# Optimization experiments

Hardware: AMD Instinct MI355X
Metric: run time of the kernel (lower is better)

The kernel has to match this reference:

```python
import jax, jax.numpy as jnp
import numpy as np

TOP_K = 5
EPS = 1e-12

def _l2norm(x, axis=-1):
    n = jnp.sqrt(jnp.sum(x * x, axis=axis, keepdims=True))
    return x / jnp.maximum(n, EPS)

def setup_inputs() -> dict:
    key = jax.random.key(0)
    ks = jax.random.split(key, 6)
    B, S, D, N = 16, 2048, 512, 200000
    return {
        "hidden_states": jax.random.normal(ks[0], (B, S, D), dtype=jnp.float32),
        "doc_embeddings": jax.random.normal(ks[1], (N, D), dtype=jnp.float32),
        "W_q": jax.random.normal(ks[2], (D, D), dtype=jnp.float32) * 0.02,
        "b_q": jnp.zeros((D,), dtype=jnp.float32),
        "W_gate": jax.random.normal(ks[3], (D, 2 * D), dtype=jnp.float32) * 0.02,
        "b_gate": jnp.zeros((D,), dtype=jnp.float32),
    }

def reference(hidden_states, doc_embeddings, W_q, b_q, W_gate, b_gate):
    B, S, D = hidden_states.shape
    # set_doc_embeddings: cosine metric normalizes doc table once
    docs = _l2norm(doc_embeddings, axis=1)          # [N, D]
    # forward: mean-pool query, linear encode
    query = hidden_states.mean(axis=1)              # [B, D]
    query = query @ W_q.T + b_q                     # torch Linear: x @ W^T + b
    # cosine similarity scan over full corpus
    q = _l2norm(query, axis=1)                      # [B, D]
    scores_full = q @ docs.T                        # [B, N]  (memory-bound scan)
    top_scores, indices = jax.lax.top_k(scores_full, TOP_K)  # [B, K], [B, K]
    # fuse context (gate method)
    retrieved = docs[indices]                       # [B, K, D] gather
    weights = jax.nn.softmax(top_scores, axis=1)    # [B, K]
    context = jnp.einsum('bk,bkd->bd', weights, retrieved)   # [B, D]
    context_exp = jnp.broadcast_to(context[:, None, :], (B, S, D))
    combined = jnp.concatenate([hidden_states, context_exp], axis=-1)  # [B, S, 2D]
    gate = jax.nn.sigmoid(combined @ W_gate.T + b_gate)       # [B, S, D]
    fused = gate * hidden_states + (1.0 - gate) * context_exp
    return top_scores, indices, fused
```

## Files before the change

kernel.cpp:

```cpp
#include <hip/hip_runtime.h>
#include <hip/hip_bf16.h>
#include <math.h>

#define BB 16
#define SS 2048
#define DD 512
#define NDOCS 200000
#define TOPK 5
#define EPSN 1e-12f
#define NEG_INF (-3.0e38f)

#define TILE_N 128
#define KC 32
#define NCHUNK (DD / KC)
#define NBLK3 ((NDOCS + TILE_N - 1) / TILE_N)

typedef short s16x8 __attribute__((ext_vector_type(8)));
typedef float f32x4 __attribute__((ext_vector_type(4)));

__device__ __forceinline__ short f2bf(float f) {
    __bf16 b = (__bf16)f;
    short s;
    __builtin_memcpy(&s, &b, 2);
    return s;
}

__device__ __forceinline__ void gload_lds16(const void* g, void* l) {
    __builtin_amdgcn_global_load_lds(
        (const __attribute__((address_space(1))) void*)g,
        (__attribute__((address_space(3))) void*)l, 16, 0, 0);
}

__global__ __launch_bounds__(128) void k1_mean_partial(
    const float* __restrict__ hs, float* __restrict__ partial) {
    int b = blockIdx.y, sc = blockIdx.x;
    int t = threadIdx.x;
    const float4* src = (const float4*)(hs + (size_t)(b * SS + sc * 64) * DD);
    float4 acc = {0.f, 0.f, 0.f, 0.f};
    for (int s = 0; s < 64; ++s) {
        float4 v = src[(size_t)s * 128 + t];
        acc.x += v.x; acc.y += v.y; acc.z += v.z; acc.w += v.w;
    }
    ((float4*)partial)[(size_t)(sc * BB + b) * 128 + t] = acc;
}

__global__ __launch_bounds__(128) void k1b_mean_reduce(
    const float* __restrict__ partial, float* __restrict__ mean) {
    int b = blockIdx.y, jc = blockIdx.x;
    int j = jc * 128 + threadIdx.x;
    float s = 0.f;
    for (int c = 0; c < 32; ++c) s += partial[(size_t)(c * BB + b) * DD + j];
    mean[(size_t)b * DD + j] = s * (1.0f / 2048.0f);
}

__global__ __launch_bounds__(256) void k2a_q_gemv(
    const float* __restrict__ mean, const float* __restrict__ Wq,
    const float* __restrict__ bq, float* __restrict__ qtmp) {
    int b = blockIdx.y, jc = blockIdx.x;
    int t = threadIdx.x;
    int r = t >> 4, c = t & 15;
    int row = jc * 16 + r;
    const float4* wr = (const float4*)(Wq + (size_t)row * DD);
    const float4* mv = (const float4*)(mean + (size_t)b * DD);
    float acc = 0.f;
#pragma unroll
    for (int it = 0; it < 8; ++it) {
        int k4 = c + it * 16;
        float4 w = wr[k4], m = mv[k4];
        acc = fmaf(w.x, m.x, acc); acc = fmaf(w.y, m.y, acc);
        acc = fmaf(w.z, m.z, acc); acc = fmaf(w.w, m.w, acc);
    }
#pragma unroll
    for (int m = 1; m < 16; m <<= 1) acc += __shfl_xor(acc, m);
    if (c == 0) qtmp[(size_t)b * DD + row] = acc + bq[row];
}

__global__ __launch_bounds__(256) void k2b_q_norm(
    const float* __restrict__ qtmp, float* __restrict__ qv) {
    int b = blockIdx.x, t = threadIdx.x;
    __shared__ float red[4];
    float a0 = qtmp[(size_t)b * DD + t];
    float a1 = qtmp[(size_t)b * DD + t + 256];
    float ss = a0 * a0 + a1 * a1;
#pragma unroll
    for (int m = 1; m < 64; m <<= 1) ss += __shfl_xor(ss, m);
    if ((t & 63) == 0) red[t >> 6] = ss;
    __syncthreads();
    float inv = 1.0f / fmaxf(sqrtf(red[0] + red[1] + red[2] + red[3]), EPSN);
    qv[(size_t)b * DD + t] = a0 * inv;
    qv[(size_t)b * DD + t + 256] = a1 * inv;
}

__global__ __launch_bounds__(256) void k2c_qsplit(
    const float* __restrict__ qv, short* __restrict__ qsplit) {
    int b = blockIdx.x, t = threadIdx.x;
#pragma unroll
    for (int kk = 0; kk < 2; ++kk) {
        int k = t + kk * 256;
        float f = qv[(size_t)b * DD + k];
        unsigned u = __float_as_uint(f);
        short hi = (short)(u >> 16);
        float r = f - __uint_as_float(u & 0xFFFF0000u);
        short lo = f2bf(r);
        int slot = k >> 3, j = k & 7;
        int off = b * 512 + ((slot ^ (b & 7)) << 3) + j;
        qsplit[off] = hi;
        qsplit[8192 + off] = lo;
    }
}

__global__ __launch_bounds__(256) void k3_scores(
    const float* __restrict__ docs, const short* __restrict__ qsplit,
    float* __restrict__ cand_s, int* __restrict__ cand_i) {
    __shared__ float4 Et[2][TILE_N * 8];
    __shared__ short qS[2 * 8192];

    int t = threadIdx.x;
    int w = t >> 6, lane = t & 63;
    int bq = lane & 15, kg = lane >> 4;
    int blk = blockIdx.x;
    long tileBase = (long)blk * TILE_N;

#pragma unroll
    for (int j = 0; j < 8; ++j) {
        int u = ((w * 8 + j) << 6) + lane;
        gload_lds16(qsplit + (size_t)u * 8, (void*)&qS[(w * 8 + j) * 512]);
    }

    auto stage = [&](int c, int buf) {
#pragma unroll
        for (int j = 0; j < 4; ++j) {
            int u = ((w * 4 + j) << 6) + lane;
            int n = u >> 3, slot = u & 7;
            int k4src = slot ^ (n & 7);
            long row = tileBase + n;
            if (row > NDOCS - 1) row = NDOCS - 1;
            gload_lds16(docs + row * (long)DD + c * KC + k4src * 4,
                        (void*)&Et[buf][(w * 4 + j) * 64]);
        }
    };

    f32x4 acc[2], n1[2], n2[2];
#pragma unroll
    for (int f = 0; f < 2; ++f) {
        acc[f] = (f32x4){0.f, 0.f, 0.f, 0.f};
        n1[f]  = (f32x4){0.f, 0.f, 0.f, 0.f};
        n2[f]  = (f32x4){0.f, 0.f, 0.f, 0.f};
    }

    stage(0, 0);
    for (int c = 0; c < NCHUNK; ++c) {
        __syncthreads();
        if (c + 1 < NCHUNK) stage(c + 1, (c + 1) & 1);

        int qphys = ((c * 4 + kg) ^ (bq & 7)) << 3;
        s16x8 qh = *(const s16x8*)&qS[bq * 512 + qphys];
        s16x8 ql = *(const s16x8*)&qS[8192 + bq * 512 + qphys];

        const float4* Eb = &Et[c & 1][0];
#pragma unroll
        for (int f = 0; f < 2; ++f) {
            int d = (w << 5) + (f << 4) + bq;
            int base = d << 3;
            float4 e0 = Eb[base + ((kg * 2) ^ (d & 7))];
            float4 e1 = Eb[base + ((kg * 2 + 1) ^ (d & 7))];
            float ef[8] = {e0.x, e0.y, e0.z, e0.w, e1.x, e1.y, e1.z, e1.w};
            s16x8 ah, al;
#pragma unroll
            for (int i = 0; i < 8; ++i) {
                unsigned u = __float_as_uint(ef[i]);
                ah[i] = (short)(u >> 16);
                al[i] = f2bf(ef[i] - __uint_as_float(u & 0xFFFF0000u));
            }
            acc[f] = __builtin_amdgcn_mfma_f32_16x16x32_bf16(ah, qh, acc[f], 0, 0, 0);
            acc[f] = __builtin_amdgcn_mfma_f32_16x16x32_bf16(ah, ql, acc[f], 0, 0, 0);
            acc[f] = __builtin_amdgcn_mfma_f32_16x16x32_bf16(al, qh, acc[f], 0, 0, 0);
            n1[f]  = __builtin_amdgcn_mfma_f32_16x16x32_bf16(ah, ah, n1[f], 0, 0, 0);
            n2[f]  = __builtin_amdgcn_mfma_f32_16x16x32_bf16(ah, al, n2[f], 0, 0, 0);
        }
    }

    float* Sb = (float*)&Et[0][0];
#pragma unroll
    for (int f = 0; f < 2; ++f) {
        int rd = bq & 3;
        float nd = n1[f][rd] + 2.0f * n2[f][rd];
        float invn = 1.0f / fmaxf(sqrtf(nd), EPSN);
#pragma unroll
        for (int r = 0; r < 4; ++r) {
            float iv = __shfl(invn, kg * 20 + r);
            int n = (w << 5) + (f << 4) + (kg << 2) + r;
            Sb[bq * TILE_N + n] = acc[f][r] * iv;
        }
    }
    __syncthreads();

    for (int jj = 0; jj < 4; ++jj) {
        int b = w * 4 + jj;
        float v[2]; int nn[2];
#pragma unroll
        for (int m = 0; m < 2; ++m) {
            int n = lane + m * 64;
            nn[m] = n;
            v[m] = (tileBase + n < NDOCS) ? Sb[b * TILE_N + n] : NEG_INF;
        }
        for (int r = 0; r < TOPK; ++r) {
            float bv = v[0]; int bi = nn[0];
            if (v[1] > bv || (v[1] == bv && nn[1] < bi)) { bv = v[1]; bi = nn[1]; }
#pragma unroll
            for (int mm = 1; mm < 64; mm <<= 1) {
                float ov = __shfl_xor(bv, mm);
                int   oi = __shfl_xor(bi, mm);
                if (ov > bv || (ov == bv && oi < bi)) { bv = ov; bi = oi; }
            }
            if (lane == 0) {
                cand_s[((long)blk * BB + b) * TOPK + r] = bv;
                cand_i[((long)blk * BB + b) * TOPK + r] = (int)(tileBase + bi);
            }
#pragma unroll
            for (int m = 0; m < 2; ++m)
                if (nn[m] == bi) v[m] = NEG_INF;
        }
    }
}

__global__ __launch_bounds__(256) void k4a_topk_ctx(
    const float* __restrict__ docs, const float* __restrict__ cand_s,
    const int* __restrict__ cand_i, float* __restrict__ ctx,
    float* __restrict__ outp) {
    int b = blockIdx.x, t = threadIdx.x;
    __shared__ float sv[256];
    __shared__ int   si[256];
    __shared__ float topv[TOPK];
    __shared__ int   topi[TOPK];
    __shared__ float red[4];
    __shared__ float nrm5[TOPK];
    __shared__ float wts[TOPK];

    float lv[TOPK]; int li[TOPK];
#pragma unroll
    for (int r = 0; r < TOPK; ++r) { lv[r] = NEG_INF; li[r] = 0x7fffffff; }

    for (int j = t; j < NBLK3 * TOPK; j += 256) {
        int blk = j / TOPK, r = j - blk * TOPK;
        float s = cand_s[(long)blk * (BB * TOPK) + b * TOPK + r];
        int  di = cand_i[(long)blk * (BB * TOPK) + b * TOPK + r];
        if (s > lv[TOPK - 1] || (s == lv[TOPK - 1] && di < li[TOPK - 1])) {
            lv[TOPK - 1] = s; li[TOPK - 1] = di;
#pragma unroll
            for (int k = TOPK - 1; k > 0; --k) {
                if (lv[k] > lv[k - 1] || (lv[k] == lv[k - 1] && li[k] < li[k - 1])) {
                    float tv = lv[k]; lv[k] = lv[k - 1]; lv[k - 1] = tv;
                    int   ti = li[k]; li[k] = li[k - 1]; li[k - 1] = ti;
                }
            }
        }
    }

    int p = 0;
    for (int r = 0; r < TOPK; ++r) {
        float hv = (p < TOPK) ? lv[p] : NEG_INF;
        int   hi = (p < TOPK) ? li[p] : 0x7fffffff;
        sv[t] = hv; si[t] = hi;
        __syncthreads();
        for (int off = 128; off > 0; off >>= 1) {
            if (t < off) {
                float ov = sv[t + off]; int oi = si[t + off];
                if (ov > sv[t] || (ov == sv[t] && oi < si[t])) { sv[t] = ov; si[t] = oi; }
            }
            __syncthreads();
        }
        if (t == 0) { topv[r] = sv[0]; topi[r] = si[0]; }
        __syncthreads();
        if (hv == topv[r] && hi == topi[r]) ++p;
        __syncthreads();
    }

    for (int r = 0; r < TOPK; ++r) {
        const float* dr = docs + (size_t)topi[r] * DD;
        float s2 = dr[t] * dr[t] + dr[t + 256] * dr[t + 256];
#pragma unroll
        for (int m = 1; m < 64; m <<= 1) s2 += __shfl_xor(s2, m);
        if ((t & 63) == 0) red[t >> 6] = s2;
        __syncthreads();
        if (t == 0) nrm5[r] = sqrtf(red[0] + red[1] + red[2] + red[3]);
        __syncthreads();
    }

    if (t == 0) {
        float m = topv[0];
        float e[TOPK], s = 0.f;
#pragma unroll
        for (int r = 0; r < TOPK; ++r) { e[r] = expf(topv[r] - m); s += e[r]; }
#pragma unroll
        for (int r = 0; r < TOPK; ++r) wts[r] = e[r] / s;
    }
    __syncthreads();

    for (int j = t; j < DD; j += 256) {
        float c = 0.f;
#pragma unroll
        for (int r = 0; r < TOPK; ++r)
            c += wts[r] * docs[(size_t)topi[r] * DD + j] / fmaxf(nrm5[r], EPSN);
        ctx[(size_t)b * DD + j] = c;
    }

    if (t < TOPK) {
        outp[b * TOPK + t] = topv[t];
        outp[BB * TOPK + b * TOPK + t] = (float)topi[t];
    }
}

__global__ __launch_bounds__(256) void k4b_ctxb_gemv(
    const float* __restrict__ ctx, const float* __restrict__ Wg,
    const float* __restrict__ bgt, float* __restrict__ ctxb) {
    int b = blockIdx.y, jc = blockIdx.x;
    int t = threadIdx.x;
    int r = t >> 4, c = t & 15;
    int row = jc * 16 + r;
    const float4* wr = (const float4*)(Wg + (size_t)row * (2 * DD) + DD);
    const float4* mv = (const float4*)(ctx + (size_t)b * DD);
    float acc = 0.f;
#pragma unroll
    for (int it = 0; it < 8; ++it) {
        int k4 = c + it * 16;
        float4 w = wr[k4], m = mv[k4];
        acc = fmaf(w.x, m.x, acc); acc = fmaf(w.y, m.y, acc);
        acc = fmaf(w.z, m.z, acc); acc = fmaf(w.w, m.w, acc);
    }
#pragma unroll
    for (int m = 1; m < 16; m <<= 1) acc += __shfl_xor(acc, m);
    if (c == 0) ctxb[(size_t)b * DD + row] = acc + bgt[row];
}

#define BK 32
__global__ __launch_bounds__(512, 2) void k5_gemm_fused(
    const float* __restrict__ hs, const float* __restrict__ Wg,
    const float* __restrict__ ctx, const float* __restrict__ ctxb,
    float* __restrict__ outF) {
    __shared__ short At[128][BK];
    __shared__ short Bt[512][BK];
    __shared__ float ctxLds[DD];
    __shared__ float ctxbLds[DD];

    int bm = blockIdx.x;
    int t = threadIdx.x;
    int wv = t >> 6, lane = t & 63, ln = lane & 15, kg = lane >> 4;
    int wm = (wv >> 2) * 64, wn = (wv & 3) * 128;
    int bbatch = bm >> 4;

    ctxLds[t]  = ctx[(size_t)bbatch * DD + t];
    ctxbLds[t] = ctxb[(size_t)bbatch * DD + t];

    float4 pf[5][2];
    auto gload = [&](int kt) {
        {
            const float* src = hs + (size_t)(bm * 128 + (t >> 2)) * DD + kt * BK + (t & 3) * 8;
            pf[0][0] = ((const float4*)src)[0];
            pf[0][1] = ((const float4*)src)[1];
        }
#pragma unroll
        for (int i = 0; i < 4; ++i) {
            int u = t + i * 512;
            const float* src = Wg + (size_t)(u >> 2) * (2 * DD) + kt * BK + (u & 3) * 8;
            pf[1 + i][0] = ((const float4*)src)[0];
            pf[1 + i][1] = ((const float4*)src)[1];
        }
    };
    auto cvt1 = [&](float4 lo, float4 hi) {
        s16x8 cv;
        cv[0] = f2bf(lo.x); cv[1] = f2bf(lo.y); cv[2] = f2bf(lo.z); cv[3] = f2bf(lo.w);
        cv[4] = f2bf(hi.x); cv[5] = f2bf(hi.y); cv[6] = f2bf(hi.z); cv[7] = f2bf(hi.w);
        return cv;
    };
    auto cvtwrite = [&]() {
        {
            int row = t >> 2, slot = t & 3;
            int sl = slot ^ ((row >> 1) & 3);
            *(s16x8*)(&At[row][sl * 8]) = cvt1(pf[0][0], pf[0][1]);
        }
#pragma unroll
        for (int i = 0; i < 4; ++i) {
            int u = t + i * 512;
            int row = u >> 2, slot = u & 3;
            int sl = slot ^ ((row >> 1) & 3);
            *(s16x8*)(&Bt[row][sl * 8]) = cvt1(pf[1 + i][0], pf[1 + i][1]);
        }
    };

    f32x4 accv[4][8];
#pragma unroll
    for (int i = 0; i < 4; ++i)
#pragma unroll
        for (int j = 0; j < 8; ++j) accv[i][j] = (f32x4){0.f, 0.f, 0.f, 0.f};

    gload(0);
    for (int kt = 0; kt < DD / BK; ++kt) {
        __syncthreads();
        cvtwrite();
        if (kt + 1 < DD / BK) gload(kt + 1);
        __syncthreads();
        s16x8 af[4], bfr[8];
#pragma unroll
        for (int mi = 0; mi < 4; ++mi) {
            int row = wm + mi * 16 + ln;
            int sl = kg ^ ((row >> 1) & 3);
            af[mi] = *(const s16x8*)&At[row][sl * 8];
        }
#pragma unroll
        for (int nj = 0; nj < 8; ++nj) {
            int row = wn + nj * 16 + ln;
            int sl = kg ^ ((row >> 1) & 3);
            bfr[nj] = *(const s16x8*)&Bt[row][sl * 8];
        }
#pragma unroll
        for (int mi = 0; mi < 4; ++mi)
#pragma unroll
            for (int nj = 0; nj < 8; ++nj)
                accv[mi][nj] = __builtin_amdgcn_mfma_f32_16x16x32_bf16(
                    af[mi], bfr[nj], accv[mi][nj], 0, 0, 0);
    }

#pragma unroll
    for (int mi = 0; mi < 4; ++mi)
#pragma unroll
        for (int nj = 0; nj < 8; ++nj)
#pragma unroll
            for (int r = 0; r < 4; ++r) {
                int ri = wm + mi * 16 + kg * 4 + r;
                int ci = wn + nj * 16 + ln;
                size_t grow = (size_t)bm * 128 + ri;
                float logit = accv[mi][nj][r] + ctxbLds[ci];
                float g = __builtin_amdgcn_rcpf(1.0f + __expf(-logit));
                float h = hs[grow * DD + ci];
                float cx = ctxLds[ci];
                outF[grow * DD + ci] = g * h + (1.0f - g) * cx;
            }
}

extern "C" void kernel_launch(void* const* d_in, const int* in_sizes, int n_in,
                              void* d_out, int out_size, void* d_ws, size_t ws_size,
                              hipStream_t stream) {
    const float* hs   = (const float*)d_in[0];
    const float* docs = (const float*)d_in[1];
    const float* Wq   = (const float*)d_in[2];
    const float* bq   = (const float*)d_in[3];
    const float* Wg   = (const float*)d_in[4];
    const float* bgt  = (const float*)d_in[5];
    float* outp = (float*)d_out;
    float* ws = (float*)d_ws;

    float* partial = ws;
    float* mean    = partial + 32 * BB * DD;
    float* qtmp    = mean + BB * DD;
    float* qv      = qtmp + BB * DD;
    float* ctx     = qv + BB * DD;
    float* ctxb    = ctx + BB * DD;
    float* cand_s  = ctxb + BB * DD;
    int*   cand_i  = (int*)(cand_s + NBLK3 * BB * TOPK);
    short* qsplit  = (short*)(cand_i + NBLK3 * BB * TOPK);

    k1_mean_partial<<<dim3(32, BB), 128, 0, stream>>>(hs, partial);
    k1b_mean_reduce<<<dim3(4, BB), 128, 0, stream>>>(partial, mean);
    k2a_q_gemv<<<dim3(32, BB), 256, 0, stream>>>(mean, Wq, bq, qtmp);
    k2b_q_norm<<<BB, 256, 0, stream>>>(qtmp, qv);
    k2c_qsplit<<<BB, 256, 0, stream>>>(qv, qsplit);
    k3_scores<<<NBLK3, 256, 0, stream>>>(docs, qsplit, cand_s, cand_i);
    k4a_topk_ctx<<<BB, 256, 0, stream>>>(docs, cand_s, cand_i, ctx, outp);
    k4b_ctxb_gemv<<<dim3(32, BB), 256, 0, stream>>>(ctx, Wg, bgt, ctxb);
    k5_gemm_fused<<<256, 512, 0, stream>>>(hs, Wg, ctx, ctxb,
                                           outp + 2 * BB * TOPK);
}
```

Baseline: 256.0 us.

## Make k3 persistent per-wave with register doc loads and running top-k

```diff
diff --git a/kernel.cpp b/kernel.cpp
--- a/kernel.cpp
+++ b/kernel.cpp
@@ -10,10 +10,8 @@
 #define EPSN 1e-12f
 #define NEG_INF (-3.0e38f)
 
-#define TILE_N 128
-#define KC 32
-#define NCHUNK (DD / KC)
-#define NBLK3 ((NDOCS + TILE_N - 1) / TILE_N)
+#define NW 4096
+#define NTILE 12500
 
 typedef short s16x8 __attribute__((ext_vector_type(8)));
 typedef float f32x4 __attribute__((ext_vector_type(4)));
@@ -109,61 +107,51 @@
     }
 }
 
-__global__ __launch_bounds__(256) void k3_scores(
+__global__ __launch_bounds__(256, 4) void k3_scores(
     const float* __restrict__ docs, const short* __restrict__ qsplit,
     float* __restrict__ cand_s, int* __restrict__ cand_i) {
-    __shared__ float4 Et[2][TILE_N * 8];
     __shared__ short qS[2 * 8192];
 
     int t = threadIdx.x;
     int w = t >> 6, lane = t & 63;
     int bq = lane & 15, kg = lane >> 4;
-    int blk = blockIdx.x;
-    long tileBase = (long)blk * TILE_N;
 
 #pragma unroll
     for (int j = 0; j < 8; ++j) {
         int u = ((w * 8 + j) << 6) + lane;
         gload_lds16(qsplit + (size_t)u * 8, (void*)&qS[(w * 8 + j) * 512]);
     }
-
-    auto stage = [&](int c, int buf) {
-#pragma unroll
-        for (int j = 0; j < 4; ++j) {
-            int u = ((w * 4 + j) << 6) + lane;
-            int n = u >> 3, slot = u & 7;
-            int k4src = slot ^ (n & 7);
-            long row = tileBase + n;
-            if (row > NDOCS - 1) row = NDOCS - 1;
-            gload_lds16(docs + row * (long)DD + c * KC + k4src * 4,
-                        (void*)&Et[buf][(w * 4 + j) * 64]);
+    __syncthreads();
+
+    int gw = blockIdx.x * 4 + w;
+
+    float lv[TOPK]; int li[TOPK];
+#pragma unroll
+    for (int r = 0; r < TOPK; ++r) { lv[r] = NEG_INF; li[r] = 0x7fffffff; }
+
+    auto ins = [&](float s, int di) {
+        if (s > lv[4] || (s == lv[4] && di < li[4])) {
+            lv[4] = s; li[4] = di;
+#pragma unroll
+            for (int k = 4; k > 0; --k) {
+                if (lv[k] > lv[k - 1] || (lv[k] == lv[k - 1] && li[k] < li[k - 1])) {
+                    float tv = lv[k]; lv[k] = lv[k - 1]; lv[k - 1] = tv;
+                    int   ti = li[k]; li[k] = li[k - 1]; li[k - 1] = ti;
+                }
+            }
         }
     };
 
-    f32x4 acc[2], n1[2], n2[2];
-#pragma unroll
-    for (int f = 0; f < 2; ++f) {
-        acc[f] = (f32x4){0.f, 0.f, 0.f, 0.f};
-        n1[f]  = (f32x4){0.f, 0.f, 0.f, 0.f};
-        n2[f]  = (f32x4){0.f, 0.f, 0.f, 0.f};
-    }
-
-    stage(0, 0);
-    for (int c = 0; c < NCHUNK; ++c) {
-        __syncthreads();
-        if (c + 1 < NCHUNK) stage(c + 1, (c + 1) & 1);
-
-        int qphys = ((c * 4 + kg) ^ (bq & 7)) << 3;
-        s16x8 qh = *(const s16x8*)&qS[bq * 512 + qphys];
-        s16x8 ql = *(const s16x8*)&qS[8192 + bq * 512 + qphys];
-
-        const float4* Eb = &Et[c & 1][0];
-#pragma unroll
-        for (int f = 0; f < 2; ++f) {
-            int d = (w << 5) + (f << 4) + bq;
-            int base = d << 3;
-            float4 e0 = Eb[base + ((kg * 2) ^ (d & 7))];
-            float4 e1 = Eb[base + ((kg * 2 + 1) ^ (d & 7))];
+    for (int tt = gw; tt < NTILE; tt += NW) {
+        const float4* dp = (const float4*)docs + (size_t)(tt * 16 + bq) * 128 + kg * 2;
+        f32x4 acc = {0.f, 0.f, 0.f, 0.f};
+        f32x4 n1  = {0.f, 0.f, 0.f, 0.f};
+        f32x4 n2  = {0.f, 0.f, 0.f, 0.f};
+
+        auto proc = [&](int c, float4 e0, float4 e1) {
+            int qoff = ((((c * 4 + kg) ^ (bq & 7)) << 3)) + bq * 512;
+            s16x8 qh = *(const s16x8*)&qS[qoff];
+            s16x8 ql = *(const s16x8*)&qS[8192 + qoff];
             float ef[8] = {e0.x, e0.y, e0.z, e0.w, e1.x, e1.y, e1.z, e1.w};
             s16x8 ah, al;
 #pragma unroll
@@ -172,54 +160,52 @@
                 ah[i] = (short)(u >> 16);
                 al[i] = f2bf(ef[i] - __uint_as_float(u & 0xFFFF0000u));
             }
-            acc[f] = __builtin_amdgcn_mfma_f32_16x16x32_bf16(ah, qh, acc[f], 0, 0, 0);
-            acc[f] = __builtin_amdgcn_mfma_f32_16x16x32_bf16(ah, ql, acc[f], 0, 0, 0);
-            acc[f] = __builtin_amdgcn_mfma_f32_16x16x32_bf16(al, qh, acc[f], 0, 0, 0);
-            n1[f]  = __builtin_amdgcn_mfma_f32_16x16x32_bf16(ah, ah, n1[f], 0, 0, 0);
-            n2[f]  = __builtin_amdgcn_mfma_f32_16x16x32_bf16(ah, al, n2[f], 0, 0, 0);
-        }
-    }
-
-    float* Sb = (float*)&Et[0][0];
-#pragma unroll
-    for (int f = 0; f < 2; ++f) {
+            acc = __builtin_amdgcn_mfma_f32_16x16x32_bf16(ah, qh, acc, 0, 0, 0);
+            acc = __builtin_amdgcn_mfma_f32_16x16x32_bf16(ah, ql, acc, 0, 0, 0);
+            acc = __builtin_amdgcn_mfma_f32_16x16x32_bf16(al, qh, acc, 0, 0, 0);
+            n1  = __builtin_amdgcn_mfma_f32_16x16x32_bf16(ah, ah, n1, 0, 0, 0);
+            n2  = __builtin_amdgcn_mfma_f32_16x16x32_bf16(ah, al, n2, 0, 0, 0);
+        };
+
+        float4 a0 = dp[0], a1 = dp[1];
+        float4 b0 = dp[8], b1 = dp[9];
+#pragma unroll
+        for (int c = 0; c < 16; c += 2) {
+            proc(c, a0, a1);
+            if (c + 2 < 16) { a0 = dp[(c + 2) * 8]; a1 = dp[(c + 2) * 8 + 1]; }
+            proc(c + 1, b0, b1);
+            if (c + 3 < 16) { b0 = dp[(c + 3) * 8]; b1 = dp[(c + 3) * 8 + 1]; }
+        }
+
         int rd = bq & 3;
-        float nd = n1[f][rd] + 2.0f * n2[f][rd];
+        float nd = n1[rd] + 2.0f * n2[rd];
         float invn = 1.0f / fmaxf(sqrtf(nd), EPSN);
 #pragma unroll
         for (int r = 0; r < 4; ++r) {
             float iv = __shfl(invn, kg * 20 + r);
-            int n = (w << 5) + (f << 4) + (kg << 2) + r;
-            Sb[bq * TILE_N + n] = acc[f][r] * iv;
-        }
-    }
-    __syncthreads();
-
-    for (int jj = 0; jj < 4; ++jj) {
-        int b = w * 4 + jj;
-        float v[2]; int nn[2];
-#pragma unroll
-        for (int m = 0; m < 2; ++m) {
-            int n = lane + m * 64;
-            nn[m] = n;
-            v[m] = (tileBase + n < NDOCS) ? Sb[b * TILE_N + n] : NEG_INF;
-        }
+            float s = acc[r] * iv;
+            int di = tt * 16 + kg * 4 + r;
+            ins(s, di);
+        }
+    }
+
+#pragma unroll
+    for (int step = 16; step <= 32; step <<= 1) {
+        float ov[TOPK]; int oi[TOPK];
+#pragma unroll
         for (int r = 0; r < TOPK; ++r) {
-            float bv = v[0]; int bi = nn[0];
-            if (v[1] > bv || (v[1] == bv && nn[1] < bi)) { bv = v[1]; bi = nn[1]; }
-#pragma unroll
-            for (int mm = 1; mm < 64; mm <<= 1) {
-                float ov = __shfl_xor(bv, mm);
-                int   oi = __shfl_xor(bi, mm);
-                if (ov > bv || (ov == bv && oi < bi)) { bv = ov; bi = oi; }
-            }
-            if (lane == 0) {
-                cand_s[((long)blk * BB + b) * TOPK + r] = bv;
-                cand_i[((long)blk * BB + b) * TOPK + r] = (int)(tileBase + bi);
-            }
-#pragma unroll
-            for (int m = 0; m < 2; ++m)
-                if (nn[m] == bi) v[m] = NEG_INF;
+            ov[r] = __shfl_xor(lv[r], step);
+            oi[r] = __shfl_xor(li[r], step);
+        }
+#pragma unroll
+        for (int r = 0; r < TOPK; ++r) ins(ov[r], oi[r]);
+    }
+
+    if (kg == 0) {
+#pragma unroll
+        for (int r = 0; r < TOPK; ++r) {
+            cand_s[((long)gw * BB + bq) * TOPK + r] = lv[r];
+            cand_i[((long)gw * BB + bq) * TOPK + r] = li[r];
         }
     }
 }
@@ -241,7 +227,7 @@
 #pragma unroll
     for (int r = 0; r < TOPK; ++r) { lv[r] = NEG_INF; li[r] = 0x7fffffff; }
 
-    for (int j = t; j < NBLK3 * TOPK; j += 256) {
+    for (int j = t; j < NW * TOPK; j += 256) {
         int blk = j / TOPK, r = j - blk * TOPK;
         float s = cand_s[(long)blk * (BB * TOPK) + b * TOPK + r];
         int  di = cand_i[(long)blk * (BB * TOPK) + b * TOPK + r];
@@ -457,15 +443,15 @@
     float* ctx     = qv + BB * DD;
     float* ctxb    = ctx + BB * DD;
     float* cand_s  = ctxb + BB * DD;
-    int*   cand_i  = (int*)(cand_s + NBLK3 * BB * TOPK);
-    short* qsplit  = (short*)(cand_i + NBLK3 * BB * TOPK);
+    int*   cand_i  = (int*)(cand_s + (size_t)NW * BB * TOPK);
+    short* qsplit  = (short*)(cand_i + (size_t)NW * BB * TOPK);
 
     k1_mean_partial<<<dim3(32, BB), 128, 0, stream>>>(hs, partial);
     k1b_mean_reduce<<<dim3(4, BB), 128, 0, stream>>>(partial, mean);
     k2a_q_gemv<<<dim3(32, BB), 256, 0, stream>>>(mean, Wq, bq, qtmp);
     k2b_q_norm<<<BB, 256, 0, stream>>>(qtmp, qv);
     k2c_qsplit<<<BB, 256, 0, stream>>>(qv, qsplit);
-    k3_scores<<<NBLK3, 256, 0, stream>>>(docs, qsplit, cand_s, cand_i);
+    k3_scores<<<NW / 4, 256, 0, stream>>>(docs, qsplit, cand_s, cand_i);
     k4a_topk_ctx<<<BB, 256, 0, stream>>>(docs, cand_s, cand_i, ctx, outp);
     k4b_ctxb_gemv<<<dim3(32, BB), 256, 0, stream>>>(ctx, Wg, bgt, ctxb);
     k5_gemm_fused<<<256, 512, 0, stream>>>(hs, Wg, ctx, ctxb,
```

New measurement: 288.9 us. 1.13x slower.
